# Kernel optimization log

Measured on AMD Instinct MI355X. Metric: run time of the kernel, lower is better.

## Reference

```python
import jax, jax.numpy as jnp
import numpy as np

NUM_HEADS = 16
LN_EPS = 1e-12


def setup_inputs() -> dict:
    key = jax.random.key(0)
    ks = jax.random.split(key, 4)
    L, B, D = 2048, 2, 1024
    x = jax.random.normal(ks[0], (L, B, D), dtype=jnp.float32)
    attention_mask = jax.random.randint(ks[1], (B, L), 0, 2, dtype=jnp.int32)
    ln_w = jnp.ones((D,), dtype=jnp.float32)
    ln_b = jnp.zeros((D,), dtype=jnp.float32)
    qkv_w = jax.random.normal(ks[2], (3 * D, D), dtype=jnp.float32) * 0.02
    qkv_b = jnp.zeros((3 * D,), dtype=jnp.float32)
    out_w = jax.random.normal(ks[3], (D, D), dtype=jnp.float32) * 0.02
    out_b = jnp.zeros((D,), dtype=jnp.float32)
    return {"x": x, "attention_mask": attention_mask, "ln_w": ln_w, "ln_b": ln_b,
            "qkv_w": qkv_w, "qkv_b": qkv_b, "out_w": out_w, "out_b": out_b}


def _layer_norm(x, w, b):
    mu = jnp.mean(x, axis=-1, keepdims=True)
    var = jnp.mean(jnp.square(x - mu), axis=-1, keepdims=True)
    return (x - mu) * jax.lax.rsqrt(var + LN_EPS) * w + b


def reference(x, attention_mask, ln_w, ln_b, qkv_w, qkv_b, out_w, out_b):
    L, B, D = x.shape
    H = NUM_HEADS
    hd = D // H
    scale = 1.0 / np.sqrt(hd).astype(np.float32)

    xn = _layer_norm(x, ln_w, ln_b)                       # (L, B, D)
    qkv = xn @ qkv_w.T + qkv_b                            # (L, B, 3D)
    q, k, v = jnp.split(qkv, 3, axis=-1)
    # (L, B, D) -> (L, B*H, hd) -> (B*H, L, hd)
    q = q.reshape(L, B * H, hd).swapaxes(0, 1)
    k = k.reshape(L, B * H, hd).swapaxes(0, 1)
    v = v.reshape(L, B * H, hd).swapaxes(0, 1)

    scores = jnp.einsum('nld,nmd->nlm', q, k) * scale     # (B*H, L, L)
    mask = jnp.broadcast_to(attention_mask[:, None, :], (B, H, L)).reshape(B * H, 1, L)
    scores = jnp.where(mask == 0, -jnp.inf, scores)
    probs = jax.nn.softmax(scores, axis=-1)               # masked cols -> 0
    # dropout prob = 0.0 -> identity
    context = jnp.einsum('nlm,nmd->nld', probs, v)        # (B*H, L, hd)
    context = context.swapaxes(0, 1).reshape(L, B, D)
    return context @ out_w.T + out_b
```

## Files before the change

kernel.cpp:

```cpp
#include <hip/hip_runtime.h>
#include <hip/hip_bf16.h>
#include <cstdint>

static constexpr int LSEQ = 2048;
static constexpr int BB   = 2;
static constexpr int DM   = 1024;
static constexpr int NHD  = 16;
static constexpr int HD   = 64;
static constexpr int ROWS = LSEQ * BB;
static constexpr int NQKV = 3 * DM;

typedef __attribute__((ext_vector_type(8))) short v8s;
typedef __attribute__((ext_vector_type(4))) float v4f;

#if __has_builtin(__builtin_amdgcn_exp2f)
#define EXP2F(x) __builtin_amdgcn_exp2f(x)
#else
#define EXP2F(x) __expf((x) * 0.69314718056f)
#endif

static constexpr float QSCALE = 0.125f * 1.44269504089f;
static constexpr float NEGM   = -10.0f * 1.44269504089f;

__device__ __forceinline__ unsigned short f2bf(float f) {
    unsigned int u = __builtin_bit_cast(unsigned int, f);
    u += 0x7fffu + ((u >> 16) & 1u);
    return (unsigned short)(u >> 16);
}

__device__ __forceinline__ void gload_lds16(const void* g, void* l) {
    auto gp = (const __attribute__((address_space(1))) unsigned int*)(uintptr_t)g;
    auto lp = (__attribute__((address_space(3))) unsigned int*)(uintptr_t)l;
    __builtin_amdgcn_global_load_lds(gp, lp, 16, 0, 0);
}

__global__ __launch_bounds__(256) void cast_w_kernel(const float* __restrict__ qkv_w,
                                                     const float* __restrict__ out_w,
                                                     unsigned short* __restrict__ wq,
                                                     unsigned short* __restrict__ wo) {
    size_t i = ((size_t)blockIdx.x * 256 + threadIdx.x) * 8;
    const float* src; unsigned short* dst; size_t off;
    if (i < (size_t)NQKV * DM) { src = qkv_w; dst = wq; off = i; }
    else                       { src = out_w; dst = wo; off = i - (size_t)NQKV * DM; }
    float4 a = *(const float4*)(src + off);
    float4 b = *(const float4*)(src + off + 4);
    ushort4 o0, o1;
    o0.x = f2bf(a.x); o0.y = f2bf(a.y); o0.z = f2bf(a.z); o0.w = f2bf(a.w);
    o1.x = f2bf(b.x); o1.y = f2bf(b.y); o1.z = f2bf(b.z); o1.w = f2bf(b.w);
    *(ushort4*)(dst + off)     = o0;
    *(ushort4*)(dst + off + 4) = o1;
}

__global__ __launch_bounds__(256) void ln_cast_kernel(const float* __restrict__ x,
                                                      const float* __restrict__ w,
                                                      const float* __restrict__ bia,
                                                      unsigned short* __restrict__ xn) {
    const int row = blockIdx.x;
    const int t = threadIdx.x;
    const float* xr = x + (size_t)row * DM;
    float4 v = ((const float4*)xr)[t];
    float s  = v.x + v.y + v.z + v.w;
    float sq = v.x*v.x + v.y*v.y + v.z*v.z + v.w*v.w;
    #pragma unroll
    for (int off = 32; off > 0; off >>= 1) {
        s  += __shfl_down(s, off);
        sq += __shfl_down(sq, off);
    }
    __shared__ float red[8];
    const int wv = t >> 6;
    if ((t & 63) == 0) { red[wv] = s; red[4 + wv] = sq; }
    __syncthreads();
    if (t == 0) {
        float S = red[0] + red[1] + red[2] + red[3];
        float Q = red[4] + red[5] + red[6] + red[7];
        float mu  = S * (1.0f / DM);
        float var = Q * (1.0f / DM) - mu * mu;
        red[0] = mu;
        red[1] = rsqrtf(var + 1e-12f);
    }
    __syncthreads();
    const float mu = red[0], rs = red[1];
    float4 wv4 = ((const float4*)w)[t];
    float4 bv4 = ((const float4*)bia)[t];
    ushort4 o;
    o.x = f2bf((v.x - mu) * rs * wv4.x + bv4.x);
    o.y = f2bf((v.y - mu) * rs * wv4.y + bv4.y);
    o.z = f2bf((v.z - mu) * rs * wv4.z + bv4.z);
    o.w = f2bf((v.w - mu) * rs * wv4.w + bv4.w);
    ((ushort4*)(xn + (size_t)row * DM))[t] = o;
}

template <int BN, int EPI>
__global__ __launch_bounds__(512) void gemm2_kernel(const unsigned short* __restrict__ A,
                                                    const unsigned short* __restrict__ Bt,
                                                    const float* __restrict__ bias,
                                                    float* __restrict__ outF,
                                                    unsigned short* __restrict__ qb,
                                                    unsigned short* __restrict__ kb,
                                                    unsigned short* __restrict__ vt,
                                                    int N) {
    constexpr int K  = DM;
    constexpr int FC = BN / 64;
    constexpr int WN = BN / 4;
    constexpr int NT = K / 64;
    __shared__ unsigned short Al[2][256 * 64];
    __shared__ unsigned short Bl[2][BN * 64];
    const int nbn = N / BN;
    const int bm = blockIdx.x / nbn;
    const int bn = blockIdx.x % nbn;
    const int tid = threadIdx.x;
    const int w = tid >> 6, lane = tid & 63;
    const int l15 = lane & 15, l4 = lane >> 4;
    const int wm = w >> 2, wn = w & 3;
    const unsigned short* Ab = A  + (size_t)bm * 256 * K;
    const unsigned short* Bb = Bt + (size_t)bn * BN * K;
    const int srow8  = lane >> 3;
    const int schunk = ((lane & 7) ^ (srow8 & 7)) * 8;
    const int swz    = l15 & 7;

    v4f acc[8][FC] = {};

    auto STAGE = [&](int buf, int t) {
        const int k0 = t * 64;
        #pragma unroll
        for (int i = 0; i < 4; ++i) {
            const int r0 = i * 64 + w * 8;
            gload_lds16(Ab + (size_t)(r0 + srow8) * K + k0 + schunk, &Al[buf][r0 * 64]);
        }
        #pragma unroll
        for (int i = 0; i < BN / 64; ++i) {
            const int r0 = i * 64 + w * 8;
            gload_lds16(Bb + (size_t)(r0 + srow8) * K + k0 + schunk, &Bl[buf][r0 * 64]);
        }
    };
    auto COMPUTE = [&](int buf) {
        #pragma unroll
        for (int ks = 0; ks < 2; ++ks) {
            v8s af[8]; v8s bf[FC];
            #pragma unroll
            for (int m = 0; m < 8; ++m) {
                const int row = wm * 128 + m * 16 + l15;
                af[m] = *(const v8s*)&Al[buf][row * 64 + ((ks * 4 + l4) ^ swz) * 8];
            }
            #pragma unroll
            for (int n = 0; n < FC; ++n) {
                const int row = wn * WN + n * 16 + l15;
                bf[n] = *(const v8s*)&Bl[buf][row * 64 + ((ks * 4 + l4) ^ swz) * 8];
            }
            #pragma unroll
            for (int m = 0; m < 8; ++m)
                #pragma unroll
                for (int n = 0; n < FC; ++n)
                    acc[m][n] = __builtin_amdgcn_mfma_f32_16x16x32_bf16(af[m], bf[n], acc[m][n], 0, 0, 0);
        }
    };

    STAGE(0, 0);
    __syncthreads();
    int cur = 0;
    for (int t = 0; t < NT - 1; ++t) {
        STAGE(cur ^ 1, t + 1);
        COMPUTE(cur);
        __syncthreads();
        cur ^= 1;
    }
    COMPUTE(cur);

    #pragma unroll
    for (int m = 0; m < 8; ++m) {
        #pragma unroll
        for (int n = 0; n < FC; ++n) {
            #pragma unroll
            for (int r = 0; r < 4; ++r) {
                const int row = bm * 256 + wm * 128 + m * 16 + l4 * 4 + r;
                const int col = bn * BN + wn * WN + n * 16 + l15;
                const float val = acc[m][n][r] + bias[col];
                if (EPI == 0) {
                    outF[(size_t)row * N + col] = val;
                } else {
                    const int lq = row >> 1, b = row & 1;
                    const int which = col >> 10, jr = col & 1023;
                    const int h = jr >> 6, d = jr & 63;
                    const int bh = b * NHD + h;
                    if (which == 0)      qb[((size_t)bh * LSEQ + lq) * HD + d] = f2bf(val * QSCALE);
                    else if (which == 1) kb[((size_t)bh * LSEQ + lq) * HD + d] = f2bf(val);
                    else                 vt[((size_t)bh * HD + d) * LSEQ + lq] = f2bf(val);
                }
            }
        }
    }
}

__global__ __launch_bounds__(256) void attn_kernel(const unsigned short* __restrict__ qbuf,
                                                   const unsigned short* __restrict__ kbuf,
                                                   const unsigned short* __restrict__ vtbuf,
                                                   const int* __restrict__ amask,
                                                   unsigned short* __restrict__ ctx) {
    __shared__ unsigned short Kl[64 * 64];
    __shared__ unsigned short Vl[64 * 64];
    __shared__ unsigned short Pl[4][2][16 * 72];
    __shared__ float mbias[64];
    const int qblk = blockIdx.x, bh = blockIdx.y;
    const int b = bh >> 4, h = bh & 15;
    const int tid = threadIdx.x;
    const int w = tid >> 6, lane = tid & 63;
    const int l15 = lane & 15, l4 = lane >> 4;
    const int q0 = qblk * 128 + w * 32;

    v8s qf[2][2];
    #pragma unroll
    for (int qt = 0; qt < 2; ++qt) {
        const unsigned short* Qp = qbuf + ((size_t)bh * LSEQ + q0 + qt * 16 + l15) * HD + l4 * 8;
        qf[qt][0] = *(const v8s*)Qp;
        qf[qt][1] = *(const v8s*)(Qp + 32);
    }
    const unsigned short* Kb = kbuf  + (size_t)bh * LSEQ * HD;
    const unsigned short* Vb = vtbuf + (size_t)bh * HD * LSEQ;

    v4f O[2][4] = {};
    float lsum[2][4] = {};

    const int srow = lane >> 3;
    const int schunk = ((lane & 7) ^ srow) * 8;
    const int swz = l15 & 7;

    for (int kv0 = 0; kv0 < LSEQ; kv0 += 64) {
        __syncthreads();
        {
            const int r0 = w * 16;
            gload_lds16(Kb + (size_t)(kv0 + r0 + srow) * HD + schunk,       &Kl[r0 * 64]);
            gload_lds16(Kb + (size_t)(kv0 + r0 + 8 + srow) * HD + schunk,   &Kl[(r0 + 8) * 64]);
            gload_lds16(Vb + (size_t)(r0 + srow) * LSEQ + kv0 + schunk,     &Vl[r0 * 64]);
            gload_lds16(Vb + (size_t)(r0 + 8 + srow) * LSEQ + kv0 + schunk, &Vl[(r0 + 8) * 64]);
            if (tid < 64) mbias[tid] = amask[b * LSEQ + kv0 + tid] ? NEGM : -1e30f;
        }
        __syncthreads();

        #pragma unroll
        for (int qt = 0; qt < 2; ++qt) {
            unsigned short* Pw = Pl[w][qt];
            #pragma unroll
            for (int n = 0; n < 4; ++n) {
                const int krow = n * 16 + l15;
                const v8s kf0 = *(const v8s*)&Kl[krow * 64 + ((0 + l4) ^ swz) * 8];
                const v8s kf1 = *(const v8s*)&Kl[krow * 64 + ((4 + l4) ^ swz) * 8];
                v4f a = {};
                a = __builtin_amdgcn_mfma_f32_16x16x32_bf16(qf[qt][0], kf0, a, 0, 0, 0);
                a = __builtin_amdgcn_mfma_f32_16x16x32_bf16(qf[qt][1], kf1, a, 0, 0, 0);
                const float mb = mbias[krow];
                #pragma unroll
                for (int r = 0; r < 4; ++r) {
                    const float p = EXP2F(a[r] + mb);
                    lsum[qt][r] += p;
                    unsigned int u = __builtin_bit_cast(unsigned int, p) + 0x8000u;
                    Pw[(l4 * 4 + r) * 72 + krow] = (unsigned short)(u >> 16);
                }
            }
        }
        asm volatile("s_waitcnt lgkmcnt(0)" ::: "memory");
        __builtin_amdgcn_sched_barrier(0);

        #pragma unroll
        for (int ks = 0; ks < 2; ++ks) {
            const v8s pa0 = *(const v8s*)&Pl[w][0][l15 * 72 + ks * 32 + l4 * 8];
            const v8s pa1 = *(const v8s*)&Pl[w][1][l15 * 72 + ks * 32 + l4 * 8];
            #pragma unroll
            for (int n = 0; n < 4; ++n) {
                const int vrow = n * 16 + l15;
                const v8s vf = *(const v8s*)&Vl[vrow * 64 + ((ks * 4 + l4) ^ swz) * 8];
                O[0][n] = __builtin_amdgcn_mfma_f32_16x16x32_bf16(pa0, vf, O[0][n], 0, 0, 0);
                O[1][n] = __builtin_amdgcn_mfma_f32_16x16x32_bf16(pa1, vf, O[1][n], 0, 0, 0);
            }
        }
    }

    #pragma unroll
    for (int qt = 0; qt < 2; ++qt)
        #pragma unroll
        for (int r = 0; r < 4; ++r) {
            #pragma unroll
            for (int off = 1; off < 16; off <<= 1)
                lsum[qt][r] += __shfl_xor(lsum[qt][r], off);
        }

    #pragma unroll
    for (int qt = 0; qt < 2; ++qt) {
        float inv[4];
        #pragma unroll
        for (int r = 0; r < 4; ++r) inv[r] = 1.0f / lsum[qt][r];
        #pragma unroll
        for (int n = 0; n < 4; ++n) {
            #pragma unroll
            for (int r = 0; r < 4; ++r) {
                const int lq = q0 + qt * 16 + l4 * 4 + r;
                const float val = O[qt][n][r] * inv[r];
                ctx[((size_t)lq * BB + b) * DM + h * HD + n * 16 + l15] = f2bf(val);
            }
        }
    }
}

extern "C" void kernel_launch(void* const* d_in, const int* in_sizes, int n_in,
                              void* d_out, int out_size, void* d_ws, size_t ws_size,
                              hipStream_t stream) {
    (void)in_sizes; (void)n_in; (void)out_size; (void)ws_size;
    const float* x     = (const float*)d_in[0];
    const int*   amask = (const int*)d_in[1];
    const float* ln_w  = (const float*)d_in[2];
    const float* ln_b  = (const float*)d_in[3];
    const float* qkv_w = (const float*)d_in[4];
    const float* qkv_b = (const float*)d_in[5];
    const float* out_w = (const float*)d_in[6];
    const float* out_b = (const float*)d_in[7];
    float* out = (float*)d_out;

    unsigned short* ws    = (unsigned short*)d_ws;
    unsigned short* xn    = ws;
    unsigned short* wq    = xn + (size_t)ROWS * DM;
    unsigned short* wo    = wq + (size_t)NQKV * DM;
    unsigned short* qbuf  = wo + (size_t)DM * DM;
    unsigned short* kbuf  = qbuf + (size_t)BB * NHD * LSEQ * HD;
    unsigned short* vtbuf = kbuf + (size_t)BB * NHD * LSEQ * HD;
    unsigned short* ctx   = vtbuf + (size_t)BB * NHD * LSEQ * HD;

    cast_w_kernel<<<2048, 256, 0, stream>>>(qkv_w, out_w, wq, wo);
    ln_cast_kernel<<<ROWS, 256, 0, stream>>>(x, ln_w, ln_b, xn);
    gemm2_kernel<192, 1><<<(ROWS / 256) * (NQKV / 192), 512, 0, stream>>>(
        xn, wq, qkv_b, nullptr, qbuf, kbuf, vtbuf, NQKV);
    attn_kernel<<<dim3(LSEQ / 128, BB * NHD), 256, 0, stream>>>(qbuf, kbuf, vtbuf, amask, ctx);
    gemm2_kernel<128, 0><<<(ROWS / 256) * (DM / 128), 512, 0, stream>>>(
        ctx, wo, out_b, out, nullptr, nullptr, nullptr, DM);
}
```

Before: 143.8 us.

## Double-buffer K/V tiles in LDS and precompute full mask bias

The attention kernel now keeps two LDS buffers for the K and V tiles. It issues async global-to-LDS loads for the next 64-key tile while computing the current one, which hides load latency and removes one barrier per iteration. The mask bias for the whole sequence is converted once into a shared array at kernel start instead of per tile. K fragments for a tile are also hoisted into registers. The cost is more LDS per block (about 58KB) and more registers, which could lower occupancy.

Result: no change. 143.6 us (-0.1%).

```diff
diff --git a/kernel.cpp b/kernel.cpp
--- a/kernel.cpp
+++ b/kernel.cpp
@@ -196,10 +196,10 @@
                                                    const unsigned short* __restrict__ vtbuf,
                                                    const int* __restrict__ amask,
                                                    unsigned short* __restrict__ ctx) {
-    __shared__ unsigned short Kl[64 * 64];
-    __shared__ unsigned short Vl[64 * 64];
+    __shared__ unsigned short Kl[2][64 * 64];
+    __shared__ unsigned short Vl[2][64 * 64];
     __shared__ unsigned short Pl[4][2][16 * 72];
-    __shared__ float mbias[64];
+    __shared__ float mb_all[LSEQ];
     const int qblk = blockIdx.x, bh = blockIdx.y;
     const int b = bh >> 4, h = bh & 15;
     const int tid = threadIdx.x;
@@ -207,6 +207,10 @@
     const int l15 = lane & 15, l4 = lane >> 4;
     const int q0 = qblk * 128 + w * 32;
 
+    #pragma unroll
+    for (int i = 0; i < LSEQ / 256; ++i)
+        mb_all[i * 256 + tid] = amask[b * LSEQ + i * 256 + tid] ? NEGM : -1e30f;
+
     v8s qf[2][2];
     #pragma unroll
     for (int qt = 0; qt < 2; ++qt) {
@@ -224,36 +228,45 @@
     const int schunk = ((lane & 7) ^ srow) * 8;
     const int swz = l15 & 7;
 
-    for (int kv0 = 0; kv0 < LSEQ; kv0 += 64) {
-        __syncthreads();
-        {
-            const int r0 = w * 16;
-            gload_lds16(Kb + (size_t)(kv0 + r0 + srow) * HD + schunk,       &Kl[r0 * 64]);
-            gload_lds16(Kb + (size_t)(kv0 + r0 + 8 + srow) * HD + schunk,   &Kl[(r0 + 8) * 64]);
-            gload_lds16(Vb + (size_t)(r0 + srow) * LSEQ + kv0 + schunk,     &Vl[r0 * 64]);
-            gload_lds16(Vb + (size_t)(r0 + 8 + srow) * LSEQ + kv0 + schunk, &Vl[(r0 + 8) * 64]);
-            if (tid < 64) mbias[tid] = amask[b * LSEQ + kv0 + tid] ? NEGM : -1e30f;
-        }
-        __syncthreads();
+    auto STAGE = [&](int buf, int kv0) {
+        const int r0 = w * 16;
+        gload_lds16(Kb + (size_t)(kv0 + r0 + srow) * HD + schunk,       &Kl[buf][r0 * 64]);
+        gload_lds16(Kb + (size_t)(kv0 + r0 + 8 + srow) * HD + schunk,   &Kl[buf][(r0 + 8) * 64]);
+        gload_lds16(Vb + (size_t)(r0 + srow) * LSEQ + kv0 + schunk,     &Vl[buf][r0 * 64]);
+        gload_lds16(Vb + (size_t)(r0 + 8 + srow) * LSEQ + kv0 + schunk, &Vl[buf][(r0 + 8) * 64]);
+    };
+
+    STAGE(0, 0);
+    __syncthreads();
+    int cur = 0;
+    for (int t = 0; t < LSEQ / 64; ++t) {
+        if (t + 1 < LSEQ / 64) STAGE(cur ^ 1, (t + 1) * 64);
+        const int kv0 = t * 64;
+
+        v8s kf[4][2];
+        float mb[4];
+        #pragma unroll
+        for (int n = 0; n < 4; ++n) {
+            const int krow = n * 16 + l15;
+            kf[n][0] = *(const v8s*)&Kl[cur][krow * 64 + ((0 + l4) ^ swz) * 8];
+            kf[n][1] = *(const v8s*)&Kl[cur][krow * 64 + ((4 + l4) ^ swz) * 8];
+            mb[n] = mb_all[kv0 + krow];
+        }
 
         #pragma unroll
         for (int qt = 0; qt < 2; ++qt) {
             unsigned short* Pw = Pl[w][qt];
             #pragma unroll
             for (int n = 0; n < 4; ++n) {
-                const int krow = n * 16 + l15;
-                const v8s kf0 = *(const v8s*)&Kl[krow * 64 + ((0 + l4) ^ swz) * 8];
-                const v8s kf1 = *(const v8s*)&Kl[krow * 64 + ((4 + l4) ^ swz) * 8];
                 v4f a = {};
-                a = __builtin_amdgcn_mfma_f32_16x16x32_bf16(qf[qt][0], kf0, a, 0, 0, 0);
-                a = __builtin_amdgcn_mfma_f32_16x16x32_bf16(qf[qt][1], kf1, a, 0, 0, 0);
-                const float mb = mbias[krow];
+                a = __builtin_amdgcn_mfma_f32_16x16x32_bf16(qf[qt][0], kf[n][0], a, 0, 0, 0);
+                a = __builtin_amdgcn_mfma_f32_16x16x32_bf16(qf[qt][1], kf[n][1], a, 0, 0, 0);
                 #pragma unroll
                 for (int r = 0; r < 4; ++r) {
-                    const float p = EXP2F(a[r] + mb);
+                    const float p = EXP2F(a[r] + mb[n]);
                     lsum[qt][r] += p;
                     unsigned int u = __builtin_bit_cast(unsigned int, p) + 0x8000u;
-                    Pw[(l4 * 4 + r) * 72 + krow] = (unsigned short)(u >> 16);
+                    Pw[(l4 * 4 + r) * 72 + n * 16 + l15] = (unsigned short)(u >> 16);
                 }
             }
         }
@@ -267,11 +280,13 @@
             #pragma unroll
             for (int n = 0; n < 4; ++n) {
                 const int vrow = n * 16 + l15;
-                const v8s vf = *(const v8s*)&Vl[vrow * 64 + ((ks * 4 + l4) ^ swz) * 8];
+                const v8s vf = *(const v8s*)&Vl[cur][vrow * 64 + ((ks * 4 + l4) ^ swz) * 8];
                 O[0][n] = __builtin_amdgcn_mfma_f32_16x16x32_bf16(pa0, vf, O[0][n], 0, 0, 0);
                 O[1][n] = __builtin_amdgcn_mfma_f32_16x16x32_bf16(pa1, vf, O[1][n], 0, 0, 0);
             }
         }
+        __syncthreads();
+        cur ^= 1;
     }
 
     #pragma unroll
```

## Halve attention query tile, remap block ids, preload full mask bias

Applied to the files above, without the earlier changes.

Each attention block now handles 64 queries instead of 128, one 16-row query tile per wave, which doubles the grid to 1024 blocks for better CU occupancy across the GPU. Block ids are remapped so that neighbouring blocks share (b,h) heads in groups, aiming at better L2/XCD locality for K/V. The mask bias for the whole sequence is precomputed into LDS once per block instead of being loaded per kv tile. In exchange, K/V tiles are loaded from global twice as often in total and each loaded tile is used by half as many MFMAs.

Result: no change. 143.2 us (-0.4%).

```diff
diff --git a/kernel.cpp b/kernel.cpp
--- a/kernel.cpp
+++ b/kernel.cpp
@@ -198,63 +198,63 @@
                                                    unsigned short* __restrict__ ctx) {
     __shared__ unsigned short Kl[64 * 64];
     __shared__ unsigned short Vl[64 * 64];
-    __shared__ unsigned short Pl[4][2][16 * 72];
-    __shared__ float mbias[64];
-    const int qblk = blockIdx.x, bh = blockIdx.y;
+    __shared__ unsigned short Pl[4][16 * 72];
+    __shared__ float mb_all[LSEQ];
+    const int id = blockIdx.x;
+    const int inner = id >> 3;
+    const int bh = (id & 7) * 4 + (inner & 3);
+    const int qblk = inner >> 2;
     const int b = bh >> 4, h = bh & 15;
     const int tid = threadIdx.x;
     const int w = tid >> 6, lane = tid & 63;
     const int l15 = lane & 15, l4 = lane >> 4;
-    const int q0 = qblk * 128 + w * 32;
-
-    v8s qf[2][2];
-    #pragma unroll
-    for (int qt = 0; qt < 2; ++qt) {
-        const unsigned short* Qp = qbuf + ((size_t)bh * LSEQ + q0 + qt * 16 + l15) * HD + l4 * 8;
-        qf[qt][0] = *(const v8s*)Qp;
-        qf[qt][1] = *(const v8s*)(Qp + 32);
-    }
+    const int q0 = qblk * 64 + w * 16;
+
+    #pragma unroll
+    for (int i = 0; i < LSEQ / 256; ++i)
+        mb_all[i * 256 + tid] = amask[b * LSEQ + i * 256 + tid] ? NEGM : -1e30f;
+
+    const unsigned short* Qp = qbuf + ((size_t)bh * LSEQ + q0 + l15) * HD + l4 * 8;
+    const v8s qf0 = *(const v8s*)Qp;
+    const v8s qf1 = *(const v8s*)(Qp + 32);
+
     const unsigned short* Kb = kbuf  + (size_t)bh * LSEQ * HD;
     const unsigned short* Vb = vtbuf + (size_t)bh * HD * LSEQ;
 
-    v4f O[2][4] = {};
-    float lsum[2][4] = {};
+    v4f O[4] = {};
+    float lsum[4] = {};
 
     const int srow = lane >> 3;
     const int schunk = ((lane & 7) ^ srow) * 8;
     const int swz = l15 & 7;
-
-    for (int kv0 = 0; kv0 < LSEQ; kv0 += 64) {
-        __syncthreads();
+    unsigned short* Pw = Pl[w];
+
+    for (int t = 0; t < LSEQ / 64; ++t) {
+        const int kv0 = t * 64;
         {
             const int r0 = w * 16;
             gload_lds16(Kb + (size_t)(kv0 + r0 + srow) * HD + schunk,       &Kl[r0 * 64]);
             gload_lds16(Kb + (size_t)(kv0 + r0 + 8 + srow) * HD + schunk,   &Kl[(r0 + 8) * 64]);
             gload_lds16(Vb + (size_t)(r0 + srow) * LSEQ + kv0 + schunk,     &Vl[r0 * 64]);
             gload_lds16(Vb + (size_t)(r0 + 8 + srow) * LSEQ + kv0 + schunk, &Vl[(r0 + 8) * 64]);
-            if (tid < 64) mbias[tid] = amask[b * LSEQ + kv0 + tid] ? NEGM : -1e30f;
         }
         __syncthreads();
 
         #pragma unroll
-        for (int qt = 0; qt < 2; ++qt) {
-            unsigned short* Pw = Pl[w][qt];
-            #pragma unroll
-            for (int n = 0; n < 4; ++n) {
-                const int krow = n * 16 + l15;
-                const v8s kf0 = *(const v8s*)&Kl[krow * 64 + ((0 + l4) ^ swz) * 8];
-                const v8s kf1 = *(const v8s*)&Kl[krow * 64 + ((4 + l4) ^ swz) * 8];
-                v4f a = {};
-                a = __builtin_amdgcn_mfma_f32_16x16x32_bf16(qf[qt][0], kf0, a, 0, 0, 0);
-                a = __builtin_amdgcn_mfma_f32_16x16x32_bf16(qf[qt][1], kf1, a, 0, 0, 0);
-                const float mb = mbias[krow];
-                #pragma unroll
-                for (int r = 0; r < 4; ++r) {
-                    const float p = EXP2F(a[r] + mb);
-                    lsum[qt][r] += p;
-                    unsigned int u = __builtin_bit_cast(unsigned int, p) + 0x8000u;
-                    Pw[(l4 * 4 + r) * 72 + krow] = (unsigned short)(u >> 16);
-                }
+        for (int n = 0; n < 4; ++n) {
+            const int krow = n * 16 + l15;
+            const v8s kf0 = *(const v8s*)&Kl[krow * 64 + ((0 + l4) ^ swz) * 8];
+            const v8s kf1 = *(const v8s*)&Kl[krow * 64 + ((4 + l4) ^ swz) * 8];
+            v4f a = {};
+            a = __builtin_amdgcn_mfma_f32_16x16x32_bf16(qf0, kf0, a, 0, 0, 0);
+            a = __builtin_amdgcn_mfma_f32_16x16x32_bf16(qf1, kf1, a, 0, 0, 0);
+            const float mb = mb_all[kv0 + krow];
+            #pragma unroll
+            for (int r = 0; r < 4; ++r) {
+                const float p = EXP2F(a[r] + mb);
+                lsum[r] += p;
+                unsigned int u = __builtin_bit_cast(unsigned int, p) + 0x8000u;
+                Pw[(l4 * 4 + r) * 72 + krow] = (unsigned short)(u >> 16);
             }
         }
         asm volatile("s_waitcnt lgkmcnt(0)" ::: "memory");
@@ -262,40 +262,34 @@
 
         #pragma unroll
         for (int ks = 0; ks < 2; ++ks) {
-            const v8s pa0 = *(const v8s*)&Pl[w][0][l15 * 72 + ks * 32 + l4 * 8];
-            const v8s pa1 = *(const v8s*)&Pl[w][1][l15 * 72 + ks * 32 + l4 * 8];
+            const v8s pa = *(const v8s*)&Pw[l15 * 72 + ks * 32 + l4 * 8];
             #pragma unroll
             for (int n = 0; n < 4; ++n) {
                 const int vrow = n * 16 + l15;
                 const v8s vf = *(const v8s*)&Vl[vrow * 64 + ((ks * 4 + l4) ^ swz) * 8];
-                O[0][n] = __builtin_amdgcn_mfma_f32_16x16x32_bf16(pa0, vf, O[0][n], 0, 0, 0);
-                O[1][n] = __builtin_amdgcn_mfma_f32_16x16x32_bf16(pa1, vf, O[1][n], 0, 0, 0);
-            }
-        }
-    }
-
-    #pragma unroll
-    for (int qt = 0; qt < 2; ++qt)
+                O[n] = __builtin_amdgcn_mfma_f32_16x16x32_bf16(pa, vf, O[n], 0, 0, 0);
+            }
+        }
+        __syncthreads();
+    }
+
+    #pragma unroll
+    for (int r = 0; r < 4; ++r) {
+        #pragma unroll
+        for (int off = 1; off < 16; off <<= 1)
+            lsum[r] += __shfl_xor(lsum[r], off);
+    }
+
+    float inv[4];
+    #pragma unroll
+    for (int r = 0; r < 4; ++r) inv[r] = 1.0f / lsum[r];
+    #pragma unroll
+    for (int n = 0; n < 4; ++n) {
         #pragma unroll
         for (int r = 0; r < 4; ++r) {
-            #pragma unroll
-            for (int off = 1; off < 16; off <<= 1)
-                lsum[qt][r] += __shfl_xor(lsum[qt][r], off);
-        }
-
-    #pragma unroll
-    for (int qt = 0; qt < 2; ++qt) {
-        float inv[4];
-        #pragma unroll
-        for (int r = 0; r < 4; ++r) inv[r] = 1.0f / lsum[qt][r];
-        #pragma unroll
-        for (int n = 0; n < 4; ++n) {
-            #pragma unroll
-            for (int r = 0; r < 4; ++r) {
-                const int lq = q0 + qt * 16 + l4 * 4 + r;
-                const float val = O[qt][n][r] * inv[r];
-                ctx[((size_t)lq * BB + b) * DM + h * HD + n * 16 + l15] = f2bf(val);
-            }
+            const int lq = q0 + l4 * 4 + r;
+            const float val = O[n][r] * inv[r];
+            ctx[((size_t)lq * BB + b) * DM + h * HD + n * 16 + l15] = f2bf(val);
         }
     }
 }
@@ -327,7 +321,7 @@
     ln_cast_kernel<<<ROWS, 256, 0, stream>>>(x, ln_w, ln_b, xn);
     gemm2_kernel<192, 1><<<(ROWS / 256) * (NQKV / 192), 512, 0, stream>>>(
         xn, wq, qkv_b, nullptr, qbuf, kbuf, vtbuf, NQKV);
-    attn_kernel<<<dim3(LSEQ / 128, BB * NHD), 256, 0, stream>>>(qbuf, kbuf, vtbuf, amask, ctx);
+    attn_kernel<<<1024, 256, 0, stream>>>(qbuf, kbuf, vtbuf, amask, ctx);
     gemm2_kernel<128, 0><<<(ROWS / 256) * (DM / 128), 512, 0, stream>>>(
         ctx, wo, out_b, out, nullptr, nullptr, nullptr, DM);
 }
```
